# Optimization experiments

Hardware: AMD Instinct MI355X
Metric: run time of the kernel (lower is better)

## Reference

```python
import jax, jax.numpy as jnp
import numpy as np

B, T, DIM, H = 32768, 28, 32, 32
N_STEPS = 10  # fixed-step RK4 replacing adaptive dopri5


def setup_inputs() -> dict:
    key = jax.random.key(0)
    ks = jax.random.split(key, 10)
    w = lambda k, shp: jax.random.normal(k, shp, jnp.float32) * 0.1
    return dict(
        inputs=jax.random.normal(ks[0], (B, T, DIM), jnp.float32),
        h0=jax.random.normal(ks[1], (B, H), jnp.float32),  # torch.randn init state
        Wih=w(ks[2], (3 * H, DIM)), Whh=w(ks[3], (3 * H, H)),
        bih=w(ks[4], (3 * H,)), bhh=w(ks[5], (3 * H,)),
        W1=w(ks[6], (H, H)), b1=w(ks[7], (H,)),
        W2=w(ks[8], (H, H)), b2=w(ks[9], (H,)),
    )


def _rhs(y, W1, b1, W2, b2):
    # odefunc: 2-layer tanh MLP, time-independent
    return jnp.tanh(y @ W1.T + b1) @ W2.T + b2


def _rk4(y, span, W1, b1, W2, b2):
    dt = span / N_STEPS
    def step(y, _):
        k1 = _rhs(y, W1, b1, W2, b2)
        k2 = _rhs(y + 0.5 * dt * k1, W1, b1, W2, b2)
        k3 = _rhs(y + 0.5 * dt * k2, W1, b1, W2, b2)
        k4 = _rhs(y + dt * k3, W1, b1, W2, b2)
        return y + (dt / 6.0) * (k1 + 2 * k2 + 2 * k3 + k4), None
    y, _ = jax.lax.scan(step, y, None, length=N_STEPS)
    return y


def _gru(x, h, Wih, Whh, bih, bhh):
    gi = x @ Wih.T + bih  # [B, 3H], PyTorch gate order: r, z, n
    gh = h @ Whh.T + bhh
    ir, iz, inn = jnp.split(gi, 3, axis=-1)
    hr, hz, hn = jnp.split(gh, 3, axis=-1)
    r = jax.nn.sigmoid(ir + hr)
    z = jax.nn.sigmoid(iz + hz)
    n = jnp.tanh(inn + r * hn)
    return (1.0 - z) * n + z * h


def reference(inputs, h0, Wih, Whh, bih, bhh, W1, b1, W2, b2):
    # initial integration over t in [0, 1]
    h = _rk4(h0, 1.0, W1, b1, W2, b2)
    # steps i = 0..26: GRU then integrate over unit interval [i+1, i+2]
    xs = jnp.swapaxes(inputs[:, : T - 1, :], 0, 1)  # [T-1, B, DIM]
    def step(h, x_t):
        h = _gru(x_t, h, Wih, Whh, bih, bhh)
        h = _rk4(h, 1.0, W1, b1, W2, b2)
        return h, None
    h, _ = jax.lax.scan(step, h, xs)
    # step i = 27: GRU then integrate over [28, 42]; odeint returns both endpoints
    h_start = _gru(inputs[:, T - 1, :], h, Wih, Whh, bih, bhh)
    h_end = _rk4(h_start, 14.0, W1, b1, W2, b2)
    return jax.nn.relu(jnp.stack([h_start, h_end], axis=0))  # [2, B, H]
```

## Files before the change

kernel.cpp:

```cpp
#include <hip/hip_runtime.h>

namespace {

constexpr int BATCH = 32768;
constexpr int TSTEPS = 28;

__device__ __forceinline__ float bpermf(int idx, float v) {
    return __int_as_float(__builtin_amdgcn_ds_bpermute(idx, __float_as_int(v)));
}

constexpr int XOR1 = 0xB1;
constexpr int XOR2 = 0x4E;

template <int CTRL>
__device__ __forceinline__ float dppf(float v) {
    return __int_as_float(__builtin_amdgcn_mov_dpp(__float_as_int(v), CTRL, 0xF, 0xF, true));
}

__device__ __forceinline__ float exp2f_fast(float x) { return __builtin_amdgcn_exp2f(x); }
__device__ __forceinline__ float rcpf_fast(float x) { return __builtin_amdgcn_rcpf(x); }

__device__ __forceinline__ float tanhf_fast(float x) {
    float e = exp2f_fast(x * 2.885390081777927f);
    return 1.0f - 2.0f * rcpf_fast(1.0f + e);
}
__device__ __forceinline__ float sigmf_fast(float x) {
    float e = exp2f_fast(x * -1.4426950408889634f);
    return rcpf_fast(1.0f + e);
}

__global__ __launch_bounds__(256) __attribute__((amdgpu_waves_per_eu(2, 2)))
void node_kernel(
    const float* __restrict__ g_inputs, const float* __restrict__ g_h0,
    const float* __restrict__ g_Wih, const float* __restrict__ g_Whh,
    const float* __restrict__ g_bih, const float* __restrict__ g_bhh,
    const float* __restrict__ g_W1, const float* __restrict__ g_b1,
    const float* __restrict__ g_W2, const float* __restrict__ g_b2,
    float* __restrict__ g_out)
{
    __shared__ __align__(16) float sWih[96 * 36];
    __shared__ __align__(16) float sWhh[96 * 36];

    const int tid = threadIdx.x;
    for (int i = tid; i < 96 * 32; i += 256) {
        int r = i >> 5, c = i & 31;
        sWih[r * 36 + c] = g_Wih[i];
        sWhh[r * 36 + c] = g_Whh[i];
    }
    __syncthreads();

    const int lane = tid & 63;
    const int wid = tid >> 6;
    const int q = lane & 3;
    const int q0 = q & 1, q1 = (q >> 1) & 1;
    const int p = ((lane >> 3) & 1) | (((lane >> 5) & 1) << 1);
    const int eloc = ((lane >> 2) & 1) | (((lane >> 4) & 1) << 1);
    const int elem = blockIdx.x * 16 + wid * 4 + eloc;
    const int off = (q0 << 1) | (q1 << 2);
    const int comp0 = ((p << 2) | q) << 1;

    int idx[4];
    {
        const int ebits = lane & 0x14;
        #pragma unroll
        for (int n = 0; n < 4; ++n) {
            int sl = n | (q0 << 3) | (q1 << 5) | ebits;
            idx[n] = sl << 2;
        }
    }

    float w1[8][8], w2[8][8];
    #pragma unroll
    for (int j = 0; j < 8; ++j) {
        const int row = 8 * p + (j ^ off);
        #pragma unroll
        for (int cb = 0; cb < 8; cb += 4) {
            float4 a = *reinterpret_cast<const float4*>(&g_W1[row * 32 + 8 * q + cb]);
            w1[j][cb] = a.x; w1[j][cb + 1] = a.y; w1[j][cb + 2] = a.z; w1[j][cb + 3] = a.w;
            float4 b = *reinterpret_cast<const float4*>(&g_W2[row * 32 + 8 * q + cb]);
            w2[j][cb] = b.x; w2[j][cb + 1] = b.y; w2[j][cb + 2] = b.z; w2[j][cb + 3] = b.w;
        }
    }

    const float b1o0 = g_b1[comp0], b1o1 = g_b1[comp0 + 1];
    const float b2o0 = g_b2[comp0], b2o1 = g_b2[comp0 + 1];
    const float br0 = g_bih[comp0] + g_bhh[comp0];
    const float br1 = g_bih[comp0 + 1] + g_bhh[comp0 + 1];
    const float bz0 = g_bih[32 + comp0] + g_bhh[32 + comp0];
    const float bz1 = g_bih[32 + comp0 + 1] + g_bhh[32 + comp0 + 1];
    const float bin0 = g_bih[64 + comp0], bin1 = g_bih[64 + comp0 + 1];
    const float bhn0 = g_bhh[64 + comp0], bhn1 = g_bhh[64 + comp0 + 1];

    float y0, y1;
    {
        float2 h = *reinterpret_cast<const float2*>(&g_h0[(size_t)elem * 32 + comp0]);
        y0 = h.x; y1 = h.y;
    }

    auto gather8 = [&](float v0, float v1, float (&in)[8]) {
        #pragma unroll
        for (int n = 0; n < 4; ++n) {
            in[2 * n]     = bpermf(idx[n], v0);
            in[2 * n + 1] = bpermf(idx[n], v1);
        }
    };

    auto reduceP = [&](float (&P)[8]) {
        P[0] += dppf<XOR2>(P[4]);
        P[1] += dppf<XOR2>(P[5]);
        P[2] += dppf<XOR2>(P[6]);
        P[3] += dppf<XOR2>(P[7]);
        P[0] += dppf<XOR1>(P[2]);
        P[1] += dppf<XOR1>(P[3]);
    };

    auto layer = [&](const float (&w)[8][8], const float (&in)[8], float& o0, float& o1) {
        float P[8];
        #pragma unroll
        for (int j = 0; j < 8; ++j) {
            float s = w[j][0] * in[0];
            #pragma unroll
            for (int cc = 1; cc < 8; ++cc) s = fmaf(w[j][cc], in[cc], s);
            P[j] = s;
        }
        reduceP(P);
        o0 = P[0]; o1 = P[1];
    };

    auto rhs = [&](float v0, float v1, float& k0, float& k1) {
        float in[8];
        gather8(v0, v1, in);
        float t0, t1;
        layer(w1, in, t0, t1);
        t0 = tanhf_fast(t0 + b1o0);
        t1 = tanhf_fast(t1 + b1o1);
        gather8(t0, t1, in);
        layer(w2, in, k0, k1);
        k0 += b2o0; k1 += b2o1;
    };

    auto rk4 = [&](float dt) {
        const float hdt = 0.5f * dt;
        const float sdt = dt * (1.0f / 6.0f);
        #pragma unroll 1
        for (int s = 0; s < 10; ++s) {
            float k0, k1, a0, a1, v0, v1;
            rhs(y0, y1, k0, k1);
            a0 = k0; a1 = k1;
            v0 = fmaf(hdt, k0, y0); v1 = fmaf(hdt, k1, y1);
            rhs(v0, v1, k0, k1);
            a0 = fmaf(2.0f, k0, a0); a1 = fmaf(2.0f, k1, a1);
            v0 = fmaf(hdt, k0, y0); v1 = fmaf(hdt, k1, y1);
            rhs(v0, v1, k0, k1);
            a0 = fmaf(2.0f, k0, a0); a1 = fmaf(2.0f, k1, a1);
            v0 = fmaf(dt, k0, y0); v1 = fmaf(dt, k1, y1);
            rhs(v0, v1, k0, k1);
            a0 += k0; a1 += k1;
            y0 = fmaf(sdt, a0, y0); y1 = fmaf(sdt, a1, y1);
        }
    };

    auto gate_dot2 = [&](int gofs, const float (&xin)[8], const float (&hin)[8],
                         float& o0, float& o1) {
        float P[8];
        #pragma unroll
        for (int j = 0; j < 8; ++j) {
            const int row = gofs + 8 * p + (j ^ off);
            const float* wi = &sWih[row * 36 + 8 * q];
            const float* wh = &sWhh[row * 36 + 8 * q];
            float4 a0v = *reinterpret_cast<const float4*>(wi);
            float4 a1v = *reinterpret_cast<const float4*>(wi + 4);
            float4 h0v = *reinterpret_cast<const float4*>(wh);
            float4 h1v = *reinterpret_cast<const float4*>(wh + 4);
            float s;
            s = a0v.x * xin[0];
            s = fmaf(a0v.y, xin[1], s);
            s = fmaf(a0v.z, xin[2], s);
            s = fmaf(a0v.w, xin[3], s);
            s = fmaf(a1v.x, xin[4], s);
            s = fmaf(a1v.y, xin[5], s);
            s = fmaf(a1v.z, xin[6], s);
            s = fmaf(a1v.w, xin[7], s);
            s = fmaf(h0v.x, hin[0], s);
            s = fmaf(h0v.y, hin[1], s);
            s = fmaf(h0v.z, hin[2], s);
            s = fmaf(h0v.w, hin[3], s);
            s = fmaf(h1v.x, hin[4], s);
            s = fmaf(h1v.y, hin[5], s);
            s = fmaf(h1v.z, hin[6], s);
            s = fmaf(h1v.w, hin[7], s);
            P[j] = s;
        }
        reduceP(P);
        o0 = P[0]; o1 = P[1];
    };

    auto gate_dot1 = [&](const float* smat, int gofs, const float (&vin)[8],
                         float& o0, float& o1) {
        float P[8];
        #pragma unroll
        for (int j = 0; j < 8; ++j) {
            const int row = gofs + 8 * p + (j ^ off);
            const float* wr = &smat[row * 36 + 8 * q];
            float4 a0v = *reinterpret_cast<const float4*>(wr);
            float4 a1v = *reinterpret_cast<const float4*>(wr + 4);
            float s;
            s = a0v.x * vin[0];
            s = fmaf(a0v.y, vin[1], s);
            s = fmaf(a0v.z, vin[2], s);
            s = fmaf(a0v.w, vin[3], s);
            s = fmaf(a1v.x, vin[4], s);
            s = fmaf(a1v.y, vin[5], s);
            s = fmaf(a1v.z, vin[6], s);
            s = fmaf(a1v.w, vin[7], s);
            P[j] = s;
        }
        reduceP(P);
        o0 = P[0]; o1 = P[1];
    };

    auto gru = [&](int t) {
        float xin[8];
        {
            const float* xp = &g_inputs[((size_t)elem * TSTEPS + t) * 32 + 8 * q];
            float4 xa = *reinterpret_cast<const float4*>(xp);
            float4 xb = *reinterpret_cast<const float4*>(xp + 4);
            xin[0] = xa.x; xin[1] = xa.y; xin[2] = xa.z; xin[3] = xa.w;
            xin[4] = xb.x; xin[5] = xb.y; xin[6] = xb.z; xin[7] = xb.w;
        }
        float hin[8];
        gather8(y0, y1, hin);
        __builtin_amdgcn_sched_barrier(0);

        float r0, r1, z0, z1, nx0, nx1, nh0, nh1;
        gate_dot2(0, xin, hin, r0, r1);
        r0 = sigmf_fast(r0 + br0);
        r1 = sigmf_fast(r1 + br1);
        __builtin_amdgcn_sched_barrier(0);
        gate_dot2(32, xin, hin, z0, z1);
        z0 = sigmf_fast(z0 + bz0);
        z1 = sigmf_fast(z1 + bz1);
        __builtin_amdgcn_sched_barrier(0);
        gate_dot1(sWih, 64, xin, nx0, nx1);
        __builtin_amdgcn_sched_barrier(0);
        gate_dot1(sWhh, 64, hin, nh0, nh1);
        __builtin_amdgcn_sched_barrier(0);
        float n0 = tanhf_fast(nx0 + bin0 + r0 * (nh0 + bhn0));
        float n1 = tanhf_fast(nx1 + bin1 + r1 * (nh1 + bhn1));
        y0 = n0 + z0 * (y0 - n0);
        y1 = n1 + z1 * (y1 - n1);
    };

    rk4(0.1f);
    #pragma unroll 1
    for (int t = 0; t < TSTEPS - 1; ++t) {
        gru(t);
        rk4(0.1f);
    }
    gru(TSTEPS - 1);
    {
        float2 hs;
        hs.x = fmaxf(y0, 0.f); hs.y = fmaxf(y1, 0.f);
        *reinterpret_cast<float2*>(&g_out[(size_t)elem * 32 + comp0]) = hs;
    }
    rk4(1.4f);
    {
        float2 he;
        he.x = fmaxf(y0, 0.f); he.y = fmaxf(y1, 0.f);
        *reinterpret_cast<float2*>(&g_out[(size_t)BATCH * 32 + (size_t)elem * 32 + comp0]) = he;
    }
}

}

extern "C" void kernel_launch(void* const* d_in, const int* in_sizes, int n_in,
                              void* d_out, int out_size, void* d_ws, size_t ws_size,
                              hipStream_t stream) {
    (void)in_sizes; (void)n_in; (void)out_size; (void)d_ws; (void)ws_size;
    const float* inputs = (const float*)d_in[0];
    const float* h0     = (const float*)d_in[1];
    const float* Wih    = (const float*)d_in[2];
    const float* Whh    = (const float*)d_in[3];
    const float* bih    = (const float*)d_in[4];
    const float* bhh    = (const float*)d_in[5];
    const float* W1     = (const float*)d_in[6];
    const float* b1     = (const float*)d_in[7];
    const float* W2     = (const float*)d_in[8];
    const float* b2     = (const float*)d_in[9];
    float* out = (float*)d_out;

    dim3 grid(BATCH / 16);
    dim3 block(256);
    hipLaunchKernelGGL(node_kernel, grid, block, 0, stream,
                       inputs, h0, Wih, Whh, bih, bhh, W1, b1, W2, b2, out);
}
```

Before: 4.188 ms.

## Remap to one hidden component per lane, halve weights per lane, raise occupancy

Changes the work decomposition so each lane owns one hidden component of one batch element (2 elements per wave) instead of two components across 4 elements, halving the per-lane register weight tiles and doubling the grid. Occupancy target is raised from 2 to 4 waves per EU, and the shared-memory weight layout switches from padded rows to an XOR swizzle to avoid bank conflicts. The aim is more latency hiding for the serial RK4 dependency chain. In exchange there are more bpermute gathers per useful FMA and twice as many waves.

Result: slower. 5.463 ms (+30.4%).

```diff
diff --git a/kernel.cpp b/kernel.cpp
--- a/kernel.cpp
+++ b/kernel.cpp
@@ -29,7 +29,7 @@
     return rcpf_fast(1.0f + e);
 }
 
-__global__ __launch_bounds__(256) __attribute__((amdgpu_waves_per_eu(2, 2)))
+__global__ __launch_bounds__(256) __attribute__((amdgpu_waves_per_eu(4, 4)))
 void node_kernel(
     const float* __restrict__ g_inputs, const float* __restrict__ g_h0,
     const float* __restrict__ g_Wih, const float* __restrict__ g_Whh,
@@ -38,105 +38,89 @@
     const float* __restrict__ g_W2, const float* __restrict__ g_b2,
     float* __restrict__ g_out)
 {
-    __shared__ __align__(16) float sWih[96 * 36];
-    __shared__ __align__(16) float sWhh[96 * 36];
+    __shared__ __align__(16) float sWih[96 * 32];
+    __shared__ __align__(16) float sWhh[96 * 32];
 
     const int tid = threadIdx.x;
     for (int i = tid; i < 96 * 32; i += 256) {
         int r = i >> 5, c = i & 31;
-        sWih[r * 36 + c] = g_Wih[i];
-        sWhh[r * 36 + c] = g_Whh[i];
+        int cs = c ^ (r & 28);
+        sWih[r * 32 + cs] = g_Wih[i];
+        sWhh[r * 32 + cs] = g_Whh[i];
     }
     __syncthreads();
 
     const int lane = tid & 63;
     const int wid = tid >> 6;
     const int q = lane & 3;
-    const int q0 = q & 1, q1 = (q >> 1) & 1;
-    const int p = ((lane >> 3) & 1) | (((lane >> 5) & 1) << 1);
-    const int eloc = ((lane >> 2) & 1) | (((lane >> 4) & 1) << 1);
-    const int elem = blockIdx.x * 16 + wid * 4 + eloc;
-    const int off = (q0 << 1) | (q1 << 2);
-    const int comp0 = ((p << 2) | q) << 1;
-
-    int idx[4];
+    const int p = (lane >> 2) & 7;
+    const int e = lane >> 5;
+    const int elem = blockIdx.x * 8 + wid * 2 + e;
+    const int cmp = (p << 2) | q;
+
+    int idx[8];
     {
-        const int ebits = lane & 0x14;
-        #pragma unroll
-        for (int n = 0; n < 4; ++n) {
-            int sl = n | (q0 << 3) | (q1 << 5) | ebits;
+        const int ebit = e << 5;
+        #pragma unroll
+        for (int n = 0; n < 8; ++n) {
+            int sl = (n & 3) | ((2 * q + (n >> 2)) << 2) | ebit;
             idx[n] = sl << 2;
         }
     }
 
-    float w1[8][8], w2[8][8];
+    float w1[4][8], w2[4][8];
     #pragma unroll
-    for (int j = 0; j < 8; ++j) {
-        const int row = 8 * p + (j ^ off);
-        #pragma unroll
-        for (int cb = 0; cb < 8; cb += 4) {
-            float4 a = *reinterpret_cast<const float4*>(&g_W1[row * 32 + 8 * q + cb]);
-            w1[j][cb] = a.x; w1[j][cb + 1] = a.y; w1[j][cb + 2] = a.z; w1[j][cb + 3] = a.w;
-            float4 b = *reinterpret_cast<const float4*>(&g_W2[row * 32 + 8 * q + cb]);
-            w2[j][cb] = b.x; w2[j][cb + 1] = b.y; w2[j][cb + 2] = b.z; w2[j][cb + 3] = b.w;
-        }
-    }
-
-    const float b1o0 = g_b1[comp0], b1o1 = g_b1[comp0 + 1];
-    const float b2o0 = g_b2[comp0], b2o1 = g_b2[comp0 + 1];
-    const float br0 = g_bih[comp0] + g_bhh[comp0];
-    const float br1 = g_bih[comp0 + 1] + g_bhh[comp0 + 1];
-    const float bz0 = g_bih[32 + comp0] + g_bhh[32 + comp0];
-    const float bz1 = g_bih[32 + comp0 + 1] + g_bhh[32 + comp0 + 1];
-    const float bin0 = g_bih[64 + comp0], bin1 = g_bih[64 + comp0 + 1];
-    const float bhn0 = g_bhh[64 + comp0], bhn1 = g_bhh[64 + comp0 + 1];
-
-    float y0, y1;
-    {
-        float2 h = *reinterpret_cast<const float2*>(&g_h0[(size_t)elem * 32 + comp0]);
-        y0 = h.x; y1 = h.y;
-    }
-
-    auto gather8 = [&](float v0, float v1, float (&in)[8]) {
-        #pragma unroll
-        for (int n = 0; n < 4; ++n) {
-            in[2 * n]     = bpermf(idx[n], v0);
-            in[2 * n + 1] = bpermf(idx[n], v1);
-        }
-    };
-
-    auto reduceP = [&](float (&P)[8]) {
-        P[0] += dppf<XOR2>(P[4]);
-        P[1] += dppf<XOR2>(P[5]);
-        P[2] += dppf<XOR2>(P[6]);
-        P[3] += dppf<XOR2>(P[7]);
-        P[0] += dppf<XOR1>(P[2]);
-        P[1] += dppf<XOR1>(P[3]);
-    };
-
-    auto layer = [&](const float (&w)[8][8], const float (&in)[8], float& o0, float& o1) {
-        float P[8];
-        #pragma unroll
-        for (int j = 0; j < 8; ++j) {
+    for (int j = 0; j < 4; ++j) {
+        const int row = 4 * p + (j ^ q);
+        float4 a = *reinterpret_cast<const float4*>(&g_W1[row * 32 + 8 * q]);
+        float4 b = *reinterpret_cast<const float4*>(&g_W1[row * 32 + 8 * q + 4]);
+        w1[j][0] = a.x; w1[j][1] = a.y; w1[j][2] = a.z; w1[j][3] = a.w;
+        w1[j][4] = b.x; w1[j][5] = b.y; w1[j][6] = b.z; w1[j][7] = b.w;
+        float4 c = *reinterpret_cast<const float4*>(&g_W2[row * 32 + 8 * q]);
+        float4 d = *reinterpret_cast<const float4*>(&g_W2[row * 32 + 8 * q + 4]);
+        w2[j][0] = c.x; w2[j][1] = c.y; w2[j][2] = c.z; w2[j][3] = c.w;
+        w2[j][4] = d.x; w2[j][5] = d.y; w2[j][6] = d.z; w2[j][7] = d.w;
+    }
+
+    const float b1o = g_b1[cmp];
+    const float b2o = g_b2[cmp];
+    const float br  = g_bih[cmp] + g_bhh[cmp];
+    const float bz  = g_bih[32 + cmp] + g_bhh[32 + cmp];
+    const float bin = g_bih[64 + cmp];
+    const float bhn = g_bhh[64 + cmp];
+
+    float y = g_h0[(size_t)elem * 32 + cmp];
+
+    auto gather8 = [&](float v, float (&in)[8]) {
+        #pragma unroll
+        for (int n = 0; n < 8; ++n) in[n] = bpermf(idx[n], v);
+    };
+
+    auto reduceP = [&](float (&P)[4]) -> float {
+        P[0] += dppf<XOR2>(P[2]);
+        P[1] += dppf<XOR2>(P[3]);
+        P[0] += dppf<XOR1>(P[1]);
+        return P[0];
+    };
+
+    auto layer = [&](const float (&w)[4][8], const float (&in)[8]) -> float {
+        float P[4];
+        #pragma unroll
+        for (int j = 0; j < 4; ++j) {
             float s = w[j][0] * in[0];
             #pragma unroll
             for (int cc = 1; cc < 8; ++cc) s = fmaf(w[j][cc], in[cc], s);
             P[j] = s;
         }
-        reduceP(P);
-        o0 = P[0]; o1 = P[1];
-    };
-
-    auto rhs = [&](float v0, float v1, float& k0, float& k1) {
+        return reduceP(P);
+    };
+
+    auto rhs = [&](float v) -> float {
         float in[8];
-        gather8(v0, v1, in);
-        float t0, t1;
-        layer(w1, in, t0, t1);
-        t0 = tanhf_fast(t0 + b1o0);
-        t1 = tanhf_fast(t1 + b1o1);
-        gather8(t0, t1, in);
-        layer(w2, in, k0, k1);
-        k0 += b2o0; k1 += b2o1;
+        gather8(v, in);
+        float t = tanhf_fast(layer(w1, in) + b1o);
+        gather8(t, in);
+        return layer(w2, in) + b2o;
     };
 
     auto rk4 = [&](float dt) {
@@ -144,43 +128,41 @@
         const float sdt = dt * (1.0f / 6.0f);
         #pragma unroll 1
         for (int s = 0; s < 10; ++s) {
-            float k0, k1, a0, a1, v0, v1;
-            rhs(y0, y1, k0, k1);
-            a0 = k0; a1 = k1;
-            v0 = fmaf(hdt, k0, y0); v1 = fmaf(hdt, k1, y1);
-            rhs(v0, v1, k0, k1);
-            a0 = fmaf(2.0f, k0, a0); a1 = fmaf(2.0f, k1, a1);
-            v0 = fmaf(hdt, k0, y0); v1 = fmaf(hdt, k1, y1);
-            rhs(v0, v1, k0, k1);
-            a0 = fmaf(2.0f, k0, a0); a1 = fmaf(2.0f, k1, a1);
-            v0 = fmaf(dt, k0, y0); v1 = fmaf(dt, k1, y1);
-            rhs(v0, v1, k0, k1);
-            a0 += k0; a1 += k1;
-            y0 = fmaf(sdt, a0, y0); y1 = fmaf(sdt, a1, y1);
-        }
-    };
-
-    auto gate_dot2 = [&](int gofs, const float (&xin)[8], const float (&hin)[8],
-                         float& o0, float& o1) {
-        float P[8];
-        #pragma unroll
-        for (int j = 0; j < 8; ++j) {
-            const int row = gofs + 8 * p + (j ^ off);
-            const float* wi = &sWih[row * 36 + 8 * q];
-            const float* wh = &sWhh[row * 36 + 8 * q];
-            float4 a0v = *reinterpret_cast<const float4*>(wi);
-            float4 a1v = *reinterpret_cast<const float4*>(wi + 4);
-            float4 h0v = *reinterpret_cast<const float4*>(wh);
-            float4 h1v = *reinterpret_cast<const float4*>(wh + 4);
+            float k1 = rhs(y);
+            float a = k1;
+            float k = rhs(fmaf(hdt, k1, y));
+            a = fmaf(2.0f, k, a);
+            k = rhs(fmaf(hdt, k, y));
+            a = fmaf(2.0f, k, a);
+            k = rhs(fmaf(dt, k, y));
+            a += k;
+            y = fmaf(sdt, a, y);
+        }
+    };
+
+    auto gate_dot2 = [&](int gofs, const float (&xin)[8], const float (&hin)[8]) -> float {
+        float P[4];
+        #pragma unroll
+        for (int j = 0; j < 4; ++j) {
+            const int row = gofs + 4 * p + (j ^ q);
+            const int swz = row & 28;
+            const int c0 = (8 * q) ^ swz;
+            const int c1 = (8 * q + 4) ^ swz;
+            const float* wi = &sWih[row * 32];
+            const float* wh = &sWhh[row * 32];
+            float4 a0 = *reinterpret_cast<const float4*>(wi + c0);
+            float4 a1 = *reinterpret_cast<const float4*>(wi + c1);
+            float4 h0v = *reinterpret_cast<const float4*>(wh + c0);
+            float4 h1v = *reinterpret_cast<const float4*>(wh + c1);
             float s;
-            s = a0v.x * xin[0];
-            s = fmaf(a0v.y, xin[1], s);
-            s = fmaf(a0v.z, xin[2], s);
-            s = fmaf(a0v.w, xin[3], s);
-            s = fmaf(a1v.x, xin[4], s);
-            s = fmaf(a1v.y, xin[5], s);
-            s = fmaf(a1v.z, xin[6], s);
-            s = fmaf(a1v.w, xin[7], s);
+            s = a0.x * xin[0];
+            s = fmaf(a0.y, xin[1], s);
+            s = fmaf(a0.z, xin[2], s);
+            s = fmaf(a0.w, xin[3], s);
+            s = fmaf(a1.x, xin[4], s);
+            s = fmaf(a1.y, xin[5], s);
+            s = fmaf(a1.z, xin[6], s);
+            s = fmaf(a1.w, xin[7], s);
             s = fmaf(h0v.x, hin[0], s);
             s = fmaf(h0v.y, hin[1], s);
             s = fmaf(h0v.z, hin[2], s);
@@ -191,32 +173,32 @@
             s = fmaf(h1v.w, hin[7], s);
             P[j] = s;
         }
-        reduceP(P);
-        o0 = P[0]; o1 = P[1];
-    };
-
-    auto gate_dot1 = [&](const float* smat, int gofs, const float (&vin)[8],
-                         float& o0, float& o1) {
-        float P[8];
-        #pragma unroll
-        for (int j = 0; j < 8; ++j) {
-            const int row = gofs + 8 * p + (j ^ off);
-            const float* wr = &smat[row * 36 + 8 * q];
-            float4 a0v = *reinterpret_cast<const float4*>(wr);
-            float4 a1v = *reinterpret_cast<const float4*>(wr + 4);
+        return reduceP(P);
+    };
+
+    auto gate_dot1 = [&](const float* smat, int gofs, const float (&vin)[8]) -> float {
+        float P[4];
+        #pragma unroll
+        for (int j = 0; j < 4; ++j) {
+            const int row = gofs + 4 * p + (j ^ q);
+            const int swz = row & 28;
+            const int c0 = (8 * q) ^ swz;
+            const int c1 = (8 * q + 4) ^ swz;
+            const float* wr = &smat[row * 32];
+            float4 a0 = *reinterpret_cast<const float4*>(wr + c0);
+            float4 a1 = *reinterpret_cast<const float4*>(wr + c1);
             float s;
-            s = a0v.x * vin[0];
-            s = fmaf(a0v.y, vin[1], s);
-            s = fmaf(a0v.z, vin[2], s);
-            s = fmaf(a0v.w, vin[3], s);
-            s = fmaf(a1v.x, vin[4], s);
-            s = fmaf(a1v.y, vin[5], s);
-            s = fmaf(a1v.z, vin[6], s);
-            s = fmaf(a1v.w, vin[7], s);
+            s = a0.x * vin[0];
+            s = fmaf(a0.y, vin[1], s);
+            s = fmaf(a0.z, vin[2], s);
+            s = fmaf(a0.w, vin[3], s);
+            s = fmaf(a1.x, vin[4], s);
+            s = fmaf(a1.y, vin[5], s);
+            s = fmaf(a1.z, vin[6], s);
+            s = fmaf(a1.w, vin[7], s);
             P[j] = s;
         }
-        reduceP(P);
-        o0 = P[0]; o1 = P[1];
+        return reduceP(P);
     };
 
     auto gru = [&](int t) {
@@ -229,26 +211,19 @@
             xin[4] = xb.x; xin[5] = xb.y; xin[6] = xb.z; xin[7] = xb.w;
         }
         float hin[8];
-        gather8(y0, y1, hin);
-        __builtin_amdgcn_sched_barrier(0);
-
-        float r0, r1, z0, z1, nx0, nx1, nh0, nh1;
-        gate_dot2(0, xin, hin, r0, r1);
-        r0 = sigmf_fast(r0 + br0);
-        r1 = sigmf_fast(r1 + br1);
-        __builtin_amdgcn_sched_barrier(0);
-        gate_dot2(32, xin, hin, z0, z1);
-        z0 = sigmf_fast(z0 + bz0);
-        z1 = sigmf_fast(z1 + bz1);
-        __builtin_amdgcn_sched_barrier(0);
-        gate_dot1(sWih, 64, xin, nx0, nx1);
-        __builtin_amdgcn_sched_barrier(0);
-        gate_dot1(sWhh, 64, hin, nh0, nh1);
-        __builtin_amdgcn_sched_barrier(0);
-        float n0 = tanhf_fast(nx0 + bin0 + r0 * (nh0 + bhn0));
-        float n1 = tanhf_fast(nx1 + bin1 + r1 * (nh1 + bhn1));
-        y0 = n0 + z0 * (y0 - n0);
-        y1 = n1 + z1 * (y1 - n1);
+        gather8(y, hin);
+        __builtin_amdgcn_sched_barrier(0);
+
+        float r = sigmf_fast(gate_dot2(0, xin, hin) + br);
+        __builtin_amdgcn_sched_barrier(0);
+        float z = sigmf_fast(gate_dot2(32, xin, hin) + bz);
+        __builtin_amdgcn_sched_barrier(0);
+        float nx = gate_dot1(sWih, 64, xin);
+        __builtin_amdgcn_sched_barrier(0);
+        float nh = gate_dot1(sWhh, 64, hin);
+        __builtin_amdgcn_sched_barrier(0);
+        float n = tanhf_fast(nx + bin + r * (nh + bhn));
+        y = n + z * (y - n);
     };
 
     rk4(0.1f);
@@ -258,17 +233,9 @@
         rk4(0.1f);
     }
     gru(TSTEPS - 1);
-    {
-        float2 hs;
-        hs.x = fmaxf(y0, 0.f); hs.y = fmaxf(y1, 0.f);
-        *reinterpret_cast<float2*>(&g_out[(size_t)elem * 32 + comp0]) = hs;
-    }
+    g_out[(size_t)elem * 32 + cmp] = fmaxf(y, 0.f);
     rk4(1.4f);
-    {
-        float2 he;
-        he.x = fmaxf(y0, 0.f); he.y = fmaxf(y1, 0.f);
-        *reinterpret_cast<float2*>(&g_out[(size_t)BATCH * 32 + (size_t)elem * 32 + comp0]) = he;
-    }
+    g_out[(size_t)BATCH * 32 + (size_t)elem * 32 + cmp] = fmaxf(y, 0.f);
 }
 
 }
@@ -289,7 +256,7 @@
     const float* b2     = (const float*)d_in[9];
     float* out = (float*)d_out;
 
-    dim3 grid(BATCH / 16);
+    dim3 grid(BATCH / 8);
     dim3 block(256);
     hipLaunchKernelGGL(node_kernel, grid, block, 0, stream,
                        inputs, h0, Wih, Whh, bih, bhh, W1, b1, W2, b2, out);
```
